# Kernel tuning notes

Measured on AMD Instinct MI355X. Metric: run time of the kernel, lower is better.

Reference implementation:

```python
import jax, jax.numpy as jnp
import numpy as np
from jax.scipy.special import logsumexp

N = 16    # taxa
K = 128   # particles
S = 512   # sites (batch == full sites)
A = 4     # alphabet (DNA)
D = 64    # embedding dim
C = 16    # site-position encoding dim
PRIOR_BL = 1.0
RATE = 1.0 / PRIOR_BL


def _log_double_factorials(n_max):
    v = np.zeros(n_max + 1)
    for i in range(2, n_max + 1):
        v[i] = v[i - 2] + np.log(i)
    return jnp.asarray(v, dtype=jnp.float32)

LOG_DF = _log_double_factorials(2 * N)


def _gather_K(arr, idx):
    return arr[jnp.arange(arr.shape[0]), idx]


def _remove2(arr_t, i1, i2):
    # drop entries i1, i2 along leading axis, preserving order (static output size t-2)
    t = arr_t.shape[0]
    ar = jnp.arange(t)
    keep = (ar != i1) & (ar != i2)
    order = jnp.argsort(~keep)[: t - 2]  # stable sort: kept entries first, in order
    return arr_t[order]


def _merge_K(arr, i1, i2, new_K):
    # replace_with_merged_K: remove the two merged subtrees, append the new one
    removed = jax.vmap(_remove2)(arr, i1, i2)
    return jnp.concatenate([removed, new_K[:, None]], axis=1)


def _stat_probs(emb_VxD, siteC_SxC, W_stat, W_site):
    logits = (emb_VxD @ W_stat)[:, None, :] + (siteC_SxC @ W_site)[None]  # V,S,A
    return jax.nn.softmax(logits, axis=-1)


def _log_P_F81(stat_KxSxA, b_K):
    # F81 rate matrix Q = pi - I  =>  P(t) = e^{-t} I + (1 - e^{-t}) pi (closed-form expm)
    e = jnp.exp(-b_K)[:, None, None, None]
    P = e * jnp.eye(A, dtype=stat_KxSxA.dtype) + (1.0 - e) * stat_KxSxA[:, :, None, :]
    return jnp.log(P + 1e-30)  # K,S,A,A


def _fel_half(logP, log_fel):
    # logsumexp_b ( logP[k,s,a,b] + log_fel[k,s,b] )
    return logsumexp(logP + log_fel[:, :, None, :], axis=-1)


def _forward(data_NxSxA, data_batched_NxSxA, site_positions_SxSfull, W_enc, W_merge, W_stat, W_pos, W_site):
    key = jax.random.key(42)
    siteC = site_positions_SxSfull @ W_pos                      # S,C
    emb0 = jnp.tanh(data_NxSxA.reshape(N, -1) @ W_enc)          # N,D (seq_encoder)
    embeddings = jnp.broadcast_to(emb0[None], (K, N, D))
    log_fel = jnp.broadcast_to(jnp.log(data_batched_NxSxA)[None], (K, N, S, A))
    leaf_counts = jnp.ones((K, N), jnp.int32)
    merge1 = jnp.zeros((K, 0), jnp.int32)
    merge2 = jnp.zeros((K, 0), jnp.int32)
    br1 = jnp.zeros((K, 0), dtype=data_NxSxA.dtype)
    br2 = jnp.zeros((K, 0), dtype=data_NxSxA.dtype)
    log_pi = jnp.zeros(K)
    log_w = jnp.zeros(K)
    log_lik = jnp.zeros(K)
    log_ws = []
    log_rate = jnp.log(jnp.asarray(RATE, data_NxSxA.dtype))
    for r in range(N - 1):
        t = N - r
        key, k1, k2, k3, k4 = jax.random.split(key, 5)
        # ---- categorical resampling ----
        idxK = jax.random.categorical(k1, log_w, shape=(K,))
        merge1, merge2 = merge1[idxK], merge2[idxK]
        br1, br2 = br1[idxK], br2[idxK]
        leaf_counts = leaf_counts[idxK]
        embeddings = embeddings[idxK]
        log_fel = log_fel[idxK]
        log_pi, log_w = log_pi[idxK], log_w[idxK]
        # ---- proposal: uniform pair + exponential branch lengths ----
        i1s, i2s = np.triu_indices(t, 1)
        npairs = len(i1s)
        p = jax.random.randint(k2, (K,), 0, npairs)
        idx1 = jnp.asarray(i1s, jnp.int32)[p]
        idx2 = jnp.asarray(i2s, jnp.int32)[p]
        b1 = jax.random.exponential(k3, (K,)) * PRIOR_BL
        b2 = jax.random.exponential(k4, (K,)) * PRIOR_BL
        log_v_plus = -jnp.log(float(npairs)) + (log_rate - RATE * b1) + (log_rate - RATE * b2)
        log_v_minus = jnp.zeros(K)
        e1, e2 = _gather_K(embeddings, idx1), _gather_K(embeddings, idx2)
        new_emb = jnp.tanh(jnp.concatenate([e1, e2], axis=-1) @ W_merge)  # K,D
        # ---- record merge history (concat_K) ----
        merge1 = jnp.concatenate([merge1, idx1[:, None]], axis=1)
        merge2 = jnp.concatenate([merge2, idx2[:, None]], axis=1)
        br1 = jnp.concatenate([br1, b1[:, None]], axis=1)
        br2 = jnp.concatenate([br2, b2[:, None]], axis=1)
        new_lc = _gather_K(leaf_counts, idx1) + _gather_K(leaf_counts, idx2)
        f1, f2 = _gather_K(log_fel, idx1), _gather_K(log_fel, idx2)
        leaf_counts = _merge_K(leaf_counts, idx1, idx2, new_lc)
        embeddings = _merge_K(embeddings, idx1, idx2, new_emb)
        # ---- Felsenstein pruning step at the new internal node ----
        stat_new = _stat_probs(new_emb, siteC, W_stat, W_site)  # K,S,A
        new_fel = _fel_half(_log_P_F81(stat_new, b1), f1) + _fel_half(_log_P_F81(stat_new, b2), f2)
        log_fel = _merge_K(log_fel, idx1, idx2, new_fel)
        # ---- forest log-likelihood and log pi ----
        tn = t - 1
        stat_all = _stat_probs(embeddings.reshape(K * tn, D), siteC, W_stat, W_site)
        log_stat = jnp.log(stat_all).reshape(K, tn, S, A)
        log_lik = jnp.sum(logsumexp(log_fel + log_stat, axis=-1), axis=(1, 2))  # K
        log_top = -jnp.sum(LOG_DF[jnp.clip(2 * leaf_counts - 3, 0)], axis=1)
        log_branch = jnp.sum(log_rate - RATE * br1, axis=1) + jnp.sum(log_rate - RATE * br2, axis=1)
        prev_log_pi = log_pi
        log_pi = log_lik + log_top + log_branch
        log_w = log_pi - prev_log_pi + log_v_minus - log_v_plus
        log_ws.append(log_w)
    log_ws = jnp.stack(log_ws)  # (N-1), K
    log_Z_SMC = jnp.sum(logsumexp(log_ws - jnp.log(float(K)), axis=1))
    best = jnp.argmax(log_lik)
    return (log_Z_SMC, log_lik, merge1[best], merge2[best], br1[best], br2[best])


def setup_inputs() -> dict:
    key = jax.random.key(0)
    ks = jax.random.split(key, 6)
    data = jax.random.uniform(ks[0], (N, S, A), minval=0.05, maxval=1.0)
    return {
        "data_NxSxA": data,
        "data_batched_NxSxA": data,
        "site_positions_SxSfull": jnp.eye(S, dtype=jnp.float32),
        "W_enc": jax.random.normal(ks[1], (S * A, D)) / float(np.sqrt(S * A)),
        "W_merge": jax.random.normal(ks[2], (2 * D, D)) / float(np.sqrt(2 * D)),
        "W_stat": jax.random.normal(ks[3], (D, A)) / float(np.sqrt(D)),
        "W_pos": jax.random.normal(ks[4], (S, C)) / float(np.sqrt(S)),
        "W_site": jax.random.normal(ks[5], (C, A)) / float(np.sqrt(C)),
    }


def reference(data_NxSxA, data_batched_NxSxA, site_positions_SxSfull, W_enc, W_merge, W_stat, W_pos, W_site):
    return _forward(data_NxSxA, data_batched_NxSxA, site_positions_SxSfull, W_enc, W_merge, W_stat, W_pos, W_site)
```

## Files before the change

### kernel.cpp

```cpp
#include <hip/hip_runtime.h>
#include <stdint.h>


#define NN 16
#define KK 128
#define SS 512
#define NR 15
#define PARTITIONABLE 1
#define TINYF 1.17549435e-38f
#define NROWS (NN + NR * KK)

__host__ __device__ __forceinline__ void tf2x32(uint32_t k0, uint32_t k1,
                                                uint32_t c0, uint32_t c1,
                                                uint32_t* o0, uint32_t* o1) {
  uint32_t ks2 = k0 ^ k1 ^ 0x1BD11BDAu;
  uint32_t x0 = c0 + k0, x1 = c1 + k1;
  uint32_t ks[3] = {k0, k1, ks2};
  const uint32_t RA[4] = {13u, 15u, 26u, 6u};
  const uint32_t RB[4] = {17u, 29u, 16u, 24u};
#pragma unroll
  for (int i = 0; i < 5; ++i) {
#pragma unroll
    for (int j = 0; j < 4; ++j) {
      uint32_t r = (i & 1) ? RB[j] : RA[j];
      x0 += x1;
      x1 = (x1 << r) | (x1 >> (32u - r));
      x1 ^= x0;
    }
    x0 += ks[(i + 1) % 3];
    x1 += ks[(i + 2) % 3] + (uint32_t)(i + 1);
  }
  *o0 = x0; *o1 = x1;
}

__device__ __forceinline__ uint32_t rbits32(uint32_t ka, uint32_t kb,
                                            uint32_t i, uint32_t total) {
#if PARTITIONABLE
  uint32_t o0, o1;
  tf2x32(ka, kb, 0u, i, &o0, &o1);
  return o0 ^ o1;
#else
  uint32_t half = total >> 1;
  uint32_t o0, o1;
  if (i < half) { tf2x32(ka, kb, i, i + half, &o0, &o1); return o0; }
  tf2x32(ka, kb, i - half, i, &o0, &o1);
  return o1;
#endif
}

__device__ __forceinline__ float bits_unif(uint32_t b) {
  return __uint_as_float((b >> 9) | 0x3f800000u) - 1.0f;
}

__device__ __forceinline__ float xla_tanh(float x) {
  float ax = fabsf(x);
  float xc = fminf(fmaxf(x, -7.90531110763549805f), 7.90531110763549805f);
  float x2 = __fmul_rn(xc, xc);
  float num = -2.76076847742355e-16f;
  num = __fadd_rn(__fmul_rn(x2, num), 2.00018790482477e-13f);
  num = __fadd_rn(__fmul_rn(x2, num), -8.60467152213735e-11f);
  num = __fadd_rn(__fmul_rn(x2, num), 5.12229709037114e-08f);
  num = __fadd_rn(__fmul_rn(x2, num), 1.48572235717979e-05f);
  num = __fadd_rn(__fmul_rn(x2, num), 6.37261928875436e-04f);
  num = __fadd_rn(__fmul_rn(x2, num), 4.89352455891786e-03f);
  num = __fmul_rn(xc, num);
  float den = 1.19825839466702e-06f;
  den = __fadd_rn(__fmul_rn(x2, den), 1.18534705686654e-04f);
  den = __fadd_rn(__fmul_rn(x2, den), 2.26843463243900e-03f);
  den = __fadd_rn(__fmul_rn(x2, den), 4.89352518554385e-03f);
  float r = __fdiv_rn(num, den);
  return (ax < 0.0004f) ? x : r;
}

__device__ __forceinline__ float fin_or0(float v) {
  return (v > -INFINITY && v < INFINITY) ? v : 0.0f;
}

__global__ void k_setup(const float* datab, const float* Wpos, const float* Wsite,
                        float* fel_pool, float* sitelog, float* logw0,
                        float* logpi0, int* lc_pool, int* ilist0, float* logdf) {
  int b = blockIdx.x, tid = threadIdx.x;
  if (b < 64) {
    int id = b * 256 + tid;
    fel_pool[id] = logf(datab[id]);
    fel_pool[16384 + id] = logf(datab[16384 + id]);
  } else if (b < 72) {
    int id = (b - 64) * 256 + tid;
    int s = id >> 2, aa = id & 3;
    float acc = 0.0f;
    for (int c = 0; c < 16; ++c) acc = fmaf(Wpos[s * 16 + c], Wsite[c * 4 + aa], acc);
    sitelog[id] = acc;
  } else {
    if (tid < KK) {
      logw0[tid] = 0.0f;
      logpi0[tid] = 0.0f;
      for (int nn2 = 0; nn2 < NN; ++nn2) ilist0[tid * 16 + nn2] = nn2;
    }
    if (tid < NN) lc_pool[tid] = 1;
    if (tid == 0) {
      double vv[33];
      vv[0] = 0.0; vv[1] = 0.0;
      for (int i = 2; i <= 32; ++i) vv[i] = vv[i - 2] + log((double)i);
      for (int i = 0; i < 33; ++i) logdf[i] = (float)vv[i];
    }
  }
}

__global__ __launch_bounds__(64) void k_emb0(const float* data, const float* Wenc,
                                             const float* Wstat, float* emb_pool,
                                             float* ew0) {
  int n = blockIdx.x, d = threadIdx.x;
  __shared__ float ne[64];
  const float* dp = data + n * 2048;
  const float* wp = Wenc + d;
  float acc = 0.0f;
#pragma unroll 32
  for (int i = 0; i < 2048; ++i) acc = fmaf(dp[i], wp[(size_t)i * 64], acc);
  float v = xla_tanh(acc);
  ne[d] = v;
  emb_pool[n * 64 + d] = v;
  __syncthreads();
  if (d < 4) {
    float s = 0.0f;
    for (int c = 0; c < 64; ++c) s = fmaf(ne[c], Wstat[c * 4 + d], s);
    ew0[n * 4 + d] = s;
  }
}

__global__ void k_leafterm(const float* fel_pool, const float* ew0,
                           const float* sitelog, float* st_pool) {
  int id = blockIdx.x * blockDim.x + threadIdx.x;
  if (id >= NN * SS) return;
  int n = id >> 9, s = id & 511;
  float lg[4], ex[4], stat[4];
  for (int a = 0; a < 4; ++a) lg[a] = __fadd_rn(ew0[n * 4 + a], sitelog[s * 4 + a]);
  float m = lg[0];
  for (int a = 1; a < 4; ++a) m = fmaxf(m, lg[a]);
  float ssum = 0.0f;
  for (int a = 0; a < 4; ++a) { ex[a] = expf(__fsub_rn(lg[a], m)); ssum = __fadd_rn(ssum, ex[a]); }
  for (int a = 0; a < 4; ++a) stat[a] = __fdiv_rn(ex[a], ssum);
  float q[4], am = -INFINITY;
  for (int a = 0; a < 4; ++a) {
    q[a] = __fadd_rn(fel_pool[n * 2048 + s * 4 + a], logf(stat[a]));
    am = fmaxf(am, q[a]);
  }
  am = fin_or0(am);
  float se = 0.0f;
  for (int a = 0; a < 4; ++a) se = __fadd_rn(se, expf(__fsub_rn(q[a], am)));
  st_pool[n * 512 + s] = __fadd_rn(logf(se), am);
}

__global__ __launch_bounds__(256) void k_round(
    uint32_t ka, uint32_t kb, uint32_t k2a, uint32_t k2b,
    uint32_t k3a, uint32_t k3b, uint32_t k4a, uint32_t k4b,
    int t, int r,
    const float* logwC, float* logwN,
    const float* logpiC, float* logpiN,
    const int* ilistC, int* ilistN,
    const int* m1C, int* m1N, const int* m2C, int* m2N,
    const float* br1C, float* br1N, const float* br2C, float* br2N,
    float* emb_pool, float* fel_pool, float* st_pool, int* lc_pool,
    const float* Wmerge, const float* Wstat, const float* sitelog,
    const float* logdf, float* logws_r, float* loglik) {
  int k = blockIdx.x, tid = threadIdx.x;
  int tn = t - 1, tn2 = t - 2;
  int newrow = NN + r * KK + k;
  __shared__ float stbuf[15 * 512];
  __shared__ float cat[128];
  __shared__ float ne[64];
  __shared__ float ewl[4];
  __shared__ float smax[4];
  __shared__ int sidx[4];
  __shared__ int sA, sI1, sI2;
  __shared__ float sB1, sB2, sLvp, sE1, sE2;
  __shared__ int ilN[16];
  __shared__ int lcb[16];
  __shared__ float brb1[15], brb2[15];

  float v = -INFINITY;
  if (tid < 128) {
    uint32_t bits = rbits32(ka, kb, (uint32_t)(k * KK + tid), KK * KK);
    float f = bits_unif(bits);
    float u = fmaxf(TINYF, __fadd_rn(f, TINYF));
    float gv = -logf(-logf(u));
    v = __fadd_rn(gv, logwC[tid]);
  } else if (tid == 128) {
    uint32_t h = rbits32(k2a, k2b, (uint32_t)k, 256u);
    uint32_t l = rbits32(k2a, k2b, (uint32_t)(128 + k), 256u);
    uint32_t span = (uint32_t)(t * (t - 1) / 2);
    uint32_t mult = 65536u % span;
    mult = (mult * mult) % span;
    uint32_t off = ((h % span) * mult + (l % span)) % span;
    int p = (int)off;
    int a1 = 0, rem = p, rl = t - 1;
    while (rem >= rl) { rem -= rl; ++a1; --rl; }
    sI1 = a1;
    sI2 = a1 + 1 + rem;
    uint32_t bb = rbits32(k3a, k3b, (uint32_t)k, 128u);
    float e1 = -log1pf(-bits_unif(bb));
    bb = rbits32(k4a, k4b, (uint32_t)k, 128u);
    float e2 = -log1pf(-bits_unif(bb));
    sB1 = e1; sB2 = e2;
    float lnp = logf((float)span);
    sLvp = __fadd_rn(__fadd_rn(-lnp, -e1), -e2);
  }
  float m = v;
  for (int d = 32; d > 0; d >>= 1) m = fmaxf(m, __shfl_xor(m, d, 64));
  int w = tid >> 6;
  if ((tid & 63) == 0) smax[w] = m;
  __syncthreads();
  float gm = fmaxf(fmaxf(smax[0], smax[1]), fmaxf(smax[2], smax[3]));
  int cand = (v == gm) ? tid : 9999;
  for (int d = 32; d > 0; d >>= 1) {
    int o = __shfl_xor(cand, d, 64);
    cand = (o < cand) ? o : cand;
  }
  if ((tid & 63) == 0) sidx[w] = cand;
  __syncthreads();
  if (tid == 0) {
    int b0 = (sidx[0] < sidx[1]) ? sidx[0] : sidx[1];
    int b1_ = (sidx[2] < sidx[3]) ? sidx[2] : sidx[3];
    sA = (b0 < b1_) ? b0 : b1_;
  }
  __syncthreads();
  int a = sA, i1 = sI1, i2 = sI2;
  int p1 = ilistC[a * 16 + i1];
  int p2 = ilistC[a * 16 + i2];

  if (tid < 64) {
    cat[tid] = emb_pool[p1 * 64 + tid];
    cat[64 + tid] = emb_pool[p2 * 64 + tid];
  } else if (tid >= 64 && tid < 80) {
    int pos = tid - 64;
    if (pos < tn2) {
      int src = pos + (pos >= i1) + (pos >= (i2 - 1));
      int row = ilistC[a * 16 + src];
      ilN[pos] = row;
      ilistN[k * 16 + pos] = row;
      lcb[pos] = lc_pool[row];
    } else if (pos == tn2) {
      ilN[pos] = newrow;
      ilistN[k * 16 + pos] = newrow;
      int lcnew = lc_pool[p1] + lc_pool[p2];
      lcb[pos] = lcnew;
      lc_pool[newrow] = lcnew;
    }
  } else if (tid >= 96 && tid < 96 + NR) {
    int j = tid - 96;
    if (j < r) {
      int v1 = m1C[a * 15 + j]; m1N[k * 15 + j] = v1;
      int v2 = m2C[a * 15 + j]; m2N[k * 15 + j] = v2;
      float w1 = br1C[a * 15 + j]; br1N[k * 15 + j] = w1; brb1[j] = w1;
      float w2 = br2C[a * 15 + j]; br2N[k * 15 + j] = w2; brb2[j] = w2;
    } else if (j == r) {
      m1N[k * 15 + r] = i1;
      m2N[k * 15 + r] = i2;
      br1N[k * 15 + r] = sB1;
      br2N[k * 15 + r] = sB2;
      brb1[r] = sB1;
      brb2[r] = sB2;
    }
  } else if (tid == 128) {
    sE1 = expf(-sB1);
  } else if (tid == 129) {
    sE2 = expf(-sB2);
  }
  __syncthreads();

  if (tid < 64) {
    float acc = 0.0f;
    for (int c = 0; c < 128; ++c) acc = fmaf(cat[c], Wmerge[c * 64 + tid], acc);
    float vv = xla_tanh(acc);
    ne[tid] = vv;
    emb_pool[newrow * 64 + tid] = vv;
  } else {
    int nf4 = tn2 * 128;
    int base = tid - 64;
    float4 tmp[10];
#pragma unroll
    for (int it = 0; it < 10; ++it) {
      int q = base + it * 192;
      if (q < nf4)
        tmp[it] = *(const float4*)(st_pool + (size_t)ilN[q >> 7] * 512 + ((q & 127) << 2));
    }
#pragma unroll
    for (int it = 0; it < 10; ++it) {
      int q = base + it * 192;
      if (q < nf4) ((float4*)stbuf)[q] = tmp[it];
    }
  }
  __syncthreads();

  if (tid < 4) {
    float s = 0.0f;
    for (int c = 0; c < 64; ++c) s = fmaf(ne[c], Wstat[c * 4 + tid], s);
    ewl[tid] = s;
  }
  __syncthreads();

  {
    float e1 = sE1, e2 = sE2;
    float om1 = __fsub_rn(1.0f, e1), om2 = __fsub_rn(1.0f, e2);
    float ewv[4];
    for (int aa = 0; aa < 4; ++aa) ewv[aa] = ewl[aa];
    for (int s = tid; s < 512; s += 256) {
      float lg[4], ex[4], stat[4];
      for (int aa = 0; aa < 4; ++aa) lg[aa] = __fadd_rn(ewv[aa], sitelog[s * 4 + aa]);
      float mm = lg[0];
      for (int aa = 1; aa < 4; ++aa) mm = fmaxf(mm, lg[aa]);
      float ssum = 0.0f;
      for (int aa = 0; aa < 4; ++aa) { ex[aa] = expf(__fsub_rn(lg[aa], mm)); ssum = __fadd_rn(ssum, ex[aa]); }
      for (int aa = 0; aa < 4; ++aa) stat[aa] = __fdiv_rn(ex[aa], ssum);
      float4 f1v = *(const float4*)(fel_pool + (size_t)p1 * 2048 + s * 4);
      float4 f2v = *(const float4*)(fel_pool + (size_t)p2 * 2048 + s * 4);
      float f1a[4] = {f1v.x, f1v.y, f1v.z, f1v.w};
      float f2a[4] = {f2v.x, f2v.y, f2v.z, f2v.w};
      float nf[4];
      for (int aa = 0; aa < 4; ++aa) {
        float q1[4], am = -INFINITY;
        for (int bb = 0; bb < 4; ++bb) {
          float P = __fadd_rn((aa == bb) ? e1 : 0.0f, __fmul_rn(om1, stat[bb]));
          float lp = logf(__fadd_rn(P, 1e-30f));
          q1[bb] = __fadd_rn(lp, f1a[bb]);
          am = fmaxf(am, q1[bb]);
        }
        am = fin_or0(am);
        float se = 0.0f;
        for (int bb = 0; bb < 4; ++bb) se = __fadd_rn(se, expf(__fsub_rn(q1[bb], am)));
        float h1 = __fadd_rn(logf(se), am);
        float q2[4], am2 = -INFINITY;
        for (int bb = 0; bb < 4; ++bb) {
          float P = __fadd_rn((aa == bb) ? e2 : 0.0f, __fmul_rn(om2, stat[bb]));
          float lp = logf(__fadd_rn(P, 1e-30f));
          q2[bb] = __fadd_rn(lp, f2a[bb]);
          am2 = fmaxf(am2, q2[bb]);
        }
        am2 = fin_or0(am2);
        float se2 = 0.0f;
        for (int bb = 0; bb < 4; ++bb) se2 = __fadd_rn(se2, expf(__fsub_rn(q2[bb], am2)));
        float h2 = __fadd_rn(logf(se2), am2);
        nf[aa] = __fadd_rn(h1, h2);
      }
      *(float4*)(fel_pool + (size_t)newrow * 2048 + s * 4) =
          make_float4(nf[0], nf[1], nf[2], nf[3]);
      float q3[4], am3 = -INFINITY;
      for (int aa = 0; aa < 4; ++aa) {
        q3[aa] = __fadd_rn(nf[aa], logf(stat[aa]));
        am3 = fmaxf(am3, q3[aa]);
      }
      am3 = fin_or0(am3);
      float se3 = 0.0f;
      for (int aa = 0; aa < 4; ++aa) se3 = __fadd_rn(se3, expf(__fsub_rn(q3[aa], am3)));
      float stv = __fadd_rn(logf(se3), am3);
      stbuf[tn2 * 512 + s] = stv;
      st_pool[(size_t)newrow * 512 + s] = stv;
    }
  }
  __syncthreads();

  if (tid == 0) {
    const float4* b4 = (const float4*)stbuf;
    int tot4 = tn * 128;
    float ll = 0.0f;
    float4 pre[8];
#pragma unroll
    for (int i = 0; i < 8; ++i) pre[i] = b4[i];
    for (int q = 8; q <= tot4; q += 8) {
      float4 cur[8];
#pragma unroll
      for (int i = 0; i < 8; ++i) cur[i] = pre[i];
      if (q < tot4) {
#pragma unroll
        for (int i = 0; i < 8; ++i) pre[i] = b4[q + i];
      }
#pragma unroll
      for (int i = 0; i < 8; ++i) {
        ll = __fadd_rn(ll, cur[i].x);
        ll = __fadd_rn(ll, cur[i].y);
        ll = __fadd_rn(ll, cur[i].z);
        ll = __fadd_rn(ll, cur[i].w);
      }
    }
    float lt = 0.0f;
    for (int pos = 0; pos < tn; ++pos) {
      int idx = 2 * lcb[pos] - 3;
      if (idx < 0) idx = 0;
      lt = __fadd_rn(lt, logdf[idx]);
    }
    lt = -lt;
    float s1 = 0.0f, s2 = 0.0f;
    for (int j = 0; j <= r; ++j) {
      s1 = __fadd_rn(s1, -brb1[j]);
      s2 = __fadd_rn(s2, -brb2[j]);
    }
    float lb = __fadd_rn(s1, s2);
    float lpi = __fadd_rn(__fadd_rn(ll, lt), lb);
    float prev = logpiC[a];
    float lw = __fsub_rn(__fadd_rn(__fsub_rn(lpi, prev), 0.0f), sLvp);
    logpiN[k] = lpi;
    logwN[k] = lw;
    logws_r[k] = lw;
    loglik[k] = ll;
  }
}

__global__ void k_final(const float* logws, const float* loglik,
                        const int* m1D, const int* m2D,
                        const float* br1D, const float* br2D, float* out) {
  int j = threadIdx.x;
  out[1 + j] = loglik[j];
  __shared__ float sm[2];
  __shared__ float ssum[2];
  __shared__ int si[2];
  float c = logf(128.0f);
  float z = 0.0f;
  for (int r = 0; r < NR; ++r) {
    float v = __fsub_rn(logws[r * KK + j], c);
    float m = v;
    for (int d = 32; d > 0; d >>= 1) m = fmaxf(m, __shfl_xor(m, d, 64));
    if ((j & 63) == 0) sm[j >> 6] = m;
    __syncthreads();
    float gm = fin_or0(fmaxf(sm[0], sm[1]));
    float e = expf(__fsub_rn(v, gm));
    for (int d = 32; d > 0; d >>= 1) e = __fadd_rn(e, __shfl_xor(e, d, 64));
    if ((j & 63) == 0) ssum[j >> 6] = e;
    __syncthreads();
    if (j == 0) z = __fadd_rn(z, __fadd_rn(logf(__fadd_rn(ssum[0], ssum[1])), gm));
    __syncthreads();
  }
  if (j == 0) out[0] = z;
  float lv = loglik[j];
  float m2 = lv;
  for (int d = 32; d > 0; d >>= 1) m2 = fmaxf(m2, __shfl_xor(m2, d, 64));
  if ((j & 63) == 0) sm[j >> 6] = m2;
  __syncthreads();
  float gm2 = fmaxf(sm[0], sm[1]);
  int cand = (lv == gm2) ? j : 9999;
  for (int d = 32; d > 0; d >>= 1) {
    int o = __shfl_xor(cand, d, 64);
    cand = (o < cand) ? o : cand;
  }
  if ((j & 63) == 0) si[j >> 6] = cand;
  __syncthreads();
  int bi = (si[0] < si[1]) ? si[0] : si[1];
  if (j < NR) {
    out[129 + j] = (float)m1D[bi * 15 + j];
    out[144 + j] = (float)m2D[bi * 15 + j];
    out[159 + j] = br1D[bi * 15 + j];
    out[174 + j] = br2D[bi * 15 + j];
  }
}

static void split5_host(uint32_t* key0, uint32_t* key1, uint32_t out[8]) {
#if PARTITIONABLE
  uint32_t nk0, nk1, o0, o1;
  tf2x32(*key0, *key1, 0u, 0u, &nk0, &nk1);
  for (int j = 1; j < 5; ++j) {
    tf2x32(*key0, *key1, 0u, (uint32_t)j, &o0, &o1);
    out[2 * (j - 1)] = o0;
    out[2 * (j - 1) + 1] = o1;
  }
  *key0 = nk0; *key1 = nk1;
#else
  uint32_t a0[5], a1[5];
  for (int i = 0; i < 5; ++i) tf2x32(*key0, *key1, (uint32_t)i, (uint32_t)(i + 5), &a0[i], &a1[i]);
  uint32_t flat[10] = {a0[0], a0[1], a0[2], a0[3], a0[4], a1[0], a1[1], a1[2], a1[3], a1[4]};
  *key0 = flat[0]; *key1 = flat[1];
  for (int j = 0; j < 8; ++j) out[j] = flat[2 + j];
#endif
}

extern "C" void kernel_launch(void* const* d_in, const int* in_sizes, int n_in,
                              void* d_out, int out_size, void* d_ws, size_t ws_size,
                              hipStream_t stream) {
  const float* data = (const float*)d_in[0];
  const float* datab = (const float*)d_in[1];
  const float* Wenc = (const float*)d_in[3];
  const float* Wmerge = (const float*)d_in[4];
  const float* Wstat = (const float*)d_in[5];
  const float* Wpos = (const float*)d_in[6];
  const float* Wsite = (const float*)d_in[7];
  float* out = (float*)d_out;

  char* base = (char*)d_ws;
  size_t off = 0;
  auto alloc = [&](size_t bytes) -> void* {
    void* p = base + off;
    off += (bytes + 255) & ~(size_t)255;
    return p;
  };
  float* fel_pool = (float*)alloc((size_t)NROWS * 2048 * 4);
  float* st_pool = (float*)alloc((size_t)NROWS * 512 * 4);
  float* emb_pool = (float*)alloc((size_t)NROWS * 64 * 4);
  int* lc_pool = (int*)alloc((size_t)NROWS * 4);
  int* ilist[2]; int* m1[2]; int* m2[2]; float* br1[2]; float* br2[2];
  float* logpi[2]; float* logw2[2];
  for (int b = 0; b < 2; ++b) ilist[b] = (int*)alloc((size_t)KK * 16 * 4);
  for (int b = 0; b < 2; ++b) m1[b] = (int*)alloc((size_t)KK * 15 * 4);
  for (int b = 0; b < 2; ++b) m2[b] = (int*)alloc((size_t)KK * 15 * 4);
  for (int b = 0; b < 2; ++b) br1[b] = (float*)alloc((size_t)KK * 15 * 4);
  for (int b = 0; b < 2; ++b) br2[b] = (float*)alloc((size_t)KK * 15 * 4);
  for (int b = 0; b < 2; ++b) logpi[b] = (float*)alloc((size_t)KK * 4);
  for (int b = 0; b < 2; ++b) logw2[b] = (float*)alloc((size_t)KK * 4);
  float* logws = (float*)alloc(NR * KK * 4);
  float* loglik = (float*)alloc(KK * 4);
  float* sitelog = (float*)alloc(SS * 4 * 4);
  float* logdf = (float*)alloc(33 * 4);
  float* ew0 = (float*)alloc(NN * 4 * 4);
  (void)ws_size; (void)in_sizes; (void)n_in; (void)out_size;

  k_setup<<<73, 256, 0, stream>>>(datab, Wpos, Wsite, fel_pool, sitelog,
                                  logw2[0], logpi[0], lc_pool, ilist[0], logdf);
  k_emb0<<<NN, 64, 0, stream>>>(data, Wenc, Wstat, emb_pool, ew0);
  k_leafterm<<<32, 256, 0, stream>>>(fel_pool, ew0, sitelog, st_pool);

  uint32_t key0 = 0u, key1 = 42u;
  for (int r = 0; r < NR; ++r) {
    uint32_t ks[8];
    split5_host(&key0, &key1, ks);
    int t = NN - r;
    int cur = r & 1, nxt = cur ^ 1;
    k_round<<<KK, 256, 0, stream>>>(
        ks[0], ks[1], ks[2], ks[3], ks[4], ks[5], ks[6], ks[7], t, r,
        logw2[cur], logw2[nxt], logpi[cur], logpi[nxt],
        ilist[cur], ilist[nxt], m1[cur], m1[nxt], m2[cur], m2[nxt],
        br1[cur], br1[nxt], br2[cur], br2[nxt],
        emb_pool, fel_pool, st_pool, lc_pool,
        Wmerge, Wstat, sitelog, logdf, logws + r * KK, loglik);
  }
  k_final<<<1, 128, 0, stream>>>(logws, loglik, m1[1], m2[1], br1[1], br2[1], out);
}
```

Measured before the change: 577.5 us.

## Overlap serial likelihood fold with site compute and hoist F81 log terms

The round kernel now launches 512 threads instead of 256. Thread 0 folds the already-gathered leaf and subtree site terms while the other threads compute the Felsenstein recursion for the new node, so only the new row is summed after the barrier. The per-site transition log values are computed once per state pair type (diagonal and off-diagonal) instead of inside the inner loop, which cuts the log calls per site. One barrier is also dropped by having every thread reduce the argmax candidates itself. In exchange, warp 0 is mostly idle during site compute, and the larger block may raise register pressure.

```diff
diff --git a/kernel.cpp b/kernel.cpp
--- a/kernel.cpp
+++ b/kernel.cpp
@@ -74,6 +74,29 @@
 
 __device__ __forceinline__ float fin_or0(float v) {
   return (v > -INFINITY && v < INFINITY) ? v : 0.0f;
+}
+
+__device__ __forceinline__ void fold8(float& ll, const float4* b4, int n4) {
+  if (n4 <= 0) return;
+  float4 pre[8];
+#pragma unroll
+  for (int i = 0; i < 8; ++i) pre[i] = b4[i];
+  for (int q = 8; q <= n4; q += 8) {
+    float4 cur[8];
+#pragma unroll
+    for (int i = 0; i < 8; ++i) cur[i] = pre[i];
+    if (q < n4) {
+#pragma unroll
+      for (int i = 0; i < 8; ++i) pre[i] = b4[q + i];
+    }
+#pragma unroll
+    for (int i = 0; i < 8; ++i) {
+      ll = __fadd_rn(ll, cur[i].x);
+      ll = __fadd_rn(ll, cur[i].y);
+      ll = __fadd_rn(ll, cur[i].z);
+      ll = __fadd_rn(ll, cur[i].w);
+    }
+  }
 }
 
 __global__ void k_setup(const float* datab, const float* Wpos, const float* Wsite,
@@ -150,7 +173,7 @@
   st_pool[n * 512 + s] = __fadd_rn(logf(se), am);
 }
 
-__global__ __launch_bounds__(256) void k_round(
+__global__ __launch_bounds__(512) void k_round(
     uint32_t ka, uint32_t kb, uint32_t k2a, uint32_t k2b,
     uint32_t k3a, uint32_t k3b, uint32_t k4a, uint32_t k4b,
     int t, int r,
@@ -169,9 +192,9 @@
   __shared__ float cat[128];
   __shared__ float ne[64];
   __shared__ float ewl[4];
-  __shared__ float smax[4];
-  __shared__ int sidx[4];
-  __shared__ int sA, sI1, sI2;
+  __shared__ float smax[8];
+  __shared__ int sidx[8];
+  __shared__ int sI1, sI2;
   __shared__ float sB1, sB2, sLvp, sE1, sE2;
   __shared__ int ilN[16];
   __shared__ int lcb[16];
@@ -209,7 +232,9 @@
   int w = tid >> 6;
   if ((tid & 63) == 0) smax[w] = m;
   __syncthreads();
-  float gm = fmaxf(fmaxf(smax[0], smax[1]), fmaxf(smax[2], smax[3]));
+  float gm = smax[0];
+#pragma unroll
+  for (int i = 1; i < 8; ++i) gm = fmaxf(gm, smax[i]);
   int cand = (v == gm) ? tid : 9999;
   for (int d = 32; d > 0; d >>= 1) {
     int o = __shfl_xor(cand, d, 64);
@@ -217,13 +242,10 @@
   }
   if ((tid & 63) == 0) sidx[w] = cand;
   __syncthreads();
-  if (tid == 0) {
-    int b0 = (sidx[0] < sidx[1]) ? sidx[0] : sidx[1];
-    int b1_ = (sidx[2] < sidx[3]) ? sidx[2] : sidx[3];
-    sA = (b0 < b1_) ? b0 : b1_;
-  }
-  __syncthreads();
-  int a = sA, i1 = sI1, i2 = sI2;
+  int a = sidx[0];
+#pragma unroll
+  for (int i = 1; i < 8; ++i) a = (sidx[i] < a) ? sidx[i] : a;
+  int i1 = sI1, i2 = sI2;
   int p1 = ilistC[a * 16 + i1];
   int p2 = ilistC[a * 16 + i2];
 
@@ -276,16 +298,16 @@
   } else {
     int nf4 = tn2 * 128;
     int base = tid - 64;
-    float4 tmp[10];
-#pragma unroll
-    for (int it = 0; it < 10; ++it) {
-      int q = base + it * 192;
+    float4 tmp[4];
+#pragma unroll
+    for (int it = 0; it < 4; ++it) {
+      int q = base + it * 448;
       if (q < nf4)
         tmp[it] = *(const float4*)(st_pool + (size_t)ilN[q >> 7] * 512 + ((q & 127) << 2));
     }
 #pragma unroll
-    for (int it = 0; it < 10; ++it) {
-      int q = base + it * 192;
+    for (int it = 0; it < 4; ++it) {
+      int q = base + it * 448;
       if (q < nf4) ((float4*)stbuf)[q] = tmp[it];
     }
   }
@@ -298,45 +320,67 @@
   }
   __syncthreads();
 
-  {
+  float ll = 0.0f;
+  if (tid == 0) {
+    fold8(ll, (const float4*)stbuf, tn2 * 128);
+  } else if (tid >= 64) {
     float e1 = sE1, e2 = sE2;
     float om1 = __fsub_rn(1.0f, e1), om2 = __fsub_rn(1.0f, e2);
     float ewv[4];
+#pragma unroll
     for (int aa = 0; aa < 4; ++aa) ewv[aa] = ewl[aa];
-    for (int s = tid; s < 512; s += 256) {
+    auto do_site = [&](int s) {
       float lg[4], ex[4], stat[4];
+#pragma unroll
       for (int aa = 0; aa < 4; ++aa) lg[aa] = __fadd_rn(ewv[aa], sitelog[s * 4 + aa]);
       float mm = lg[0];
+#pragma unroll
       for (int aa = 1; aa < 4; ++aa) mm = fmaxf(mm, lg[aa]);
       float ssum = 0.0f;
-      for (int aa = 0; aa < 4; ++aa) { ex[aa] = expf(__fsub_rn(lg[aa], mm)); ssum = __fadd_rn(ssum, ex[aa]); }
+#pragma unroll
+      for (int aa = 0; aa < 4; ++aa) {
+        ex[aa] = expf(__fsub_rn(lg[aa], mm));
+        ssum = __fadd_rn(ssum, ex[aa]);
+      }
+#pragma unroll
       for (int aa = 0; aa < 4; ++aa) stat[aa] = __fdiv_rn(ex[aa], ssum);
       float4 f1v = *(const float4*)(fel_pool + (size_t)p1 * 2048 + s * 4);
       float4 f2v = *(const float4*)(fel_pool + (size_t)p2 * 2048 + s * 4);
       float f1a[4] = {f1v.x, f1v.y, f1v.z, f1v.w};
       float f2a[4] = {f2v.x, f2v.y, f2v.z, f2v.w};
+      float lo1[4], ld1[4], lo2[4], ld2[4];
+#pragma unroll
+      for (int bb = 0; bb < 4; ++bb) {
+        float m1v = __fmul_rn(om1, stat[bb]);
+        lo1[bb] = logf(__fadd_rn(m1v, 1e-30f));
+        ld1[bb] = logf(__fadd_rn(__fadd_rn(e1, m1v), 1e-30f));
+        float m2v = __fmul_rn(om2, stat[bb]);
+        lo2[bb] = logf(__fadd_rn(m2v, 1e-30f));
+        ld2[bb] = logf(__fadd_rn(__fadd_rn(e2, m2v), 1e-30f));
+      }
       float nf[4];
+#pragma unroll
       for (int aa = 0; aa < 4; ++aa) {
         float q1[4], am = -INFINITY;
+#pragma unroll
         for (int bb = 0; bb < 4; ++bb) {
-          float P = __fadd_rn((aa == bb) ? e1 : 0.0f, __fmul_rn(om1, stat[bb]));
-          float lp = logf(__fadd_rn(P, 1e-30f));
-          q1[bb] = __fadd_rn(lp, f1a[bb]);
+          q1[bb] = __fadd_rn((aa == bb) ? ld1[bb] : lo1[bb], f1a[bb]);
           am = fmaxf(am, q1[bb]);
         }
         am = fin_or0(am);
         float se = 0.0f;
+#pragma unroll
         for (int bb = 0; bb < 4; ++bb) se = __fadd_rn(se, expf(__fsub_rn(q1[bb], am)));
         float h1 = __fadd_rn(logf(se), am);
         float q2[4], am2 = -INFINITY;
+#pragma unroll
         for (int bb = 0; bb < 4; ++bb) {
-          float P = __fadd_rn((aa == bb) ? e2 : 0.0f, __fmul_rn(om2, stat[bb]));
-          float lp = logf(__fadd_rn(P, 1e-30f));
-          q2[bb] = __fadd_rn(lp, f2a[bb]);
+          q2[bb] = __fadd_rn((aa == bb) ? ld2[bb] : lo2[bb], f2a[bb]);
           am2 = fmaxf(am2, q2[bb]);
         }
         am2 = fin_or0(am2);
         float se2 = 0.0f;
+#pragma unroll
         for (int bb = 0; bb < 4; ++bb) se2 = __fadd_rn(se2, expf(__fsub_rn(q2[bb], am2)));
         float h2 = __fadd_rn(logf(se2), am2);
         nf[aa] = __fadd_rn(h1, h2);
@@ -344,43 +388,26 @@
       *(float4*)(fel_pool + (size_t)newrow * 2048 + s * 4) =
           make_float4(nf[0], nf[1], nf[2], nf[3]);
       float q3[4], am3 = -INFINITY;
+#pragma unroll
       for (int aa = 0; aa < 4; ++aa) {
         q3[aa] = __fadd_rn(nf[aa], logf(stat[aa]));
         am3 = fmaxf(am3, q3[aa]);
       }
       am3 = fin_or0(am3);
       float se3 = 0.0f;
+#pragma unroll
       for (int aa = 0; aa < 4; ++aa) se3 = __fadd_rn(se3, expf(__fsub_rn(q3[aa], am3)));
       float stv = __fadd_rn(logf(se3), am3);
       stbuf[tn2 * 512 + s] = stv;
       st_pool[(size_t)newrow * 512 + s] = stv;
-    }
+    };
+    do_site(tid - 64);
+    if (tid >= 448) do_site(tid);
   }
   __syncthreads();
 
   if (tid == 0) {
-    const float4* b4 = (const float4*)stbuf;
-    int tot4 = tn * 128;
-    float ll = 0.0f;
-    float4 pre[8];
-#pragma unroll
-    for (int i = 0; i < 8; ++i) pre[i] = b4[i];
-    for (int q = 8; q <= tot4; q += 8) {
-      float4 cur[8];
-#pragma unroll
-      for (int i = 0; i < 8; ++i) cur[i] = pre[i];
-      if (q < tot4) {
-#pragma unroll
-        for (int i = 0; i < 8; ++i) pre[i] = b4[q + i];
-      }
-#pragma unroll
-      for (int i = 0; i < 8; ++i) {
-        ll = __fadd_rn(ll, cur[i].x);
-        ll = __fadd_rn(ll, cur[i].y);
-        ll = __fadd_rn(ll, cur[i].z);
-        ll = __fadd_rn(ll, cur[i].w);
-      }
-    }
+    fold8(ll, (const float4*)(stbuf + tn2 * 512), 128);
     float lt = 0.0f;
     for (int pos = 0; pos < tn; ++pos) {
       int idx = 2 * lcb[pos] - 3;
@@ -520,7 +547,7 @@
     split5_host(&key0, &key1, ks);
     int t = NN - r;
     int cur = r & 1, nxt = cur ^ 1;
-    k_round<<<KK, 256, 0, stream>>>(
+    k_round<<<KK, 512, 0, stream>>>(
         ks[0], ks[1], ks[2], ks[3], ks[4], ks[5], ks[6], ks[7], t, r,
         logw2[cur], logw2[nxt], logpi[cur], logpi[nxt],
         ilist[cur], ilist[nxt], m1[cur], m1[nxt], m2[cur], m2[nxt],
```

Measured after the change: 601.0 us. 1.04x slower.
